# Kernel tuning notes

Measured on AMD Instinct MI355X. Metric: run time of the kernel, lower is better.

## Reference

```python
import jax, jax.numpy as jnp
import numpy as np

D_MODEL = 1024
N_HEADS = 16
HEAD_DIM = D_MODEL // N_HEADS


def setup_inputs() -> dict:
    key = jax.random.key(0)
    ks = jax.random.split(key, 5)
    B, S = 4, 2048
    scale = 1.0 / np.sqrt(D_MODEL)
    return {
        "x": jax.random.normal(ks[0], (B, S, D_MODEL), dtype=jnp.float32),
        "wq": jax.random.normal(ks[1], (D_MODEL, D_MODEL), dtype=jnp.float32) * scale,
        "wk": jax.random.normal(ks[2], (D_MODEL, D_MODEL), dtype=jnp.float32) * scale,
        "wv": jax.random.normal(ks[3], (D_MODEL, D_MODEL), dtype=jnp.float32) * scale,
        "wo": jax.random.normal(ks[4], (D_MODEL, D_MODEL), dtype=jnp.float32) * scale,
    }


def reference(x, wq, wk, wv, wo):
    B, S, _ = x.shape
    # projections: x @ W.T, then split heads -> [B, H, S, hd]
    def split_heads(t):
        return t.reshape(B, S, N_HEADS, HEAD_DIM).transpose(0, 2, 1, 3)

    q = split_heads(x @ wq.T)
    k = split_heads(x @ wk.T)
    v = split_heads(x @ wv.T)

    # scores [B, H, S, S], causal mask, stable softmax
    score = jnp.einsum("bhqd,bhkd->bhqk", q, k) / np.sqrt(HEAD_DIM)
    causal = jnp.tril(jnp.ones((S, S), dtype=bool))
    score = jnp.where(causal, score, -jnp.inf)
    attn = jax.nn.softmax(score, axis=-1)

    out = jnp.einsum("bhqk,bhkd->bhqd", attn, v)
    out = out.transpose(0, 2, 1, 3).reshape(B, S, D_MODEL)
    return out @ wo.T
```

## Files before the change

kernel.cpp:

```cpp
#include <hip/hip_runtime.h>
#include <type_traits>


typedef unsigned short u16;
typedef __attribute__((ext_vector_type(8))) short s8;
typedef __attribute__((ext_vector_type(4))) float f4;

#if __has_builtin(__builtin_amdgcn_exp2f)
#define EXP2(x) __builtin_amdgcn_exp2f(x)
#else
#define EXP2(x) exp2f(x)
#endif

__device__ __forceinline__ u16 f2bf(float f) {
    union { float f; unsigned u; } v; v.f = f;
    unsigned r = v.u + 0x7fffu + ((v.u >> 16) & 1u);
    return (u16)(r >> 16);
}

__device__ __forceinline__ unsigned pack_bf2(float a, float b) {
    return __builtin_amdgcn_perm(__float_as_uint(b), __float_as_uint(a),
                                 0x07060302u);
}

__device__ __forceinline__ void cp16(const void* g, void* l) {
    __builtin_amdgcn_global_load_lds(
        (const __attribute__((address_space(1))) unsigned int*)g,
        (__attribute__((address_space(3))) unsigned int*)l, 16, 0, 0);
}

__device__ __forceinline__ s8 load8f(const float* p) {
    const float4 lo = *(const float4*)p;
    const float4 hi = *(const float4*)(p + 4);
    s8 r;
    r[0] = (short)f2bf(lo.x); r[1] = (short)f2bf(lo.y);
    r[2] = (short)f2bf(lo.z); r[3] = (short)f2bf(lo.w);
    r[4] = (short)f2bf(hi.x); r[5] = (short)f2bf(hi.y);
    r[6] = (short)f2bf(hi.z); r[7] = (short)f2bf(hi.w);
    return r;
}

__global__ __launch_bounds__(256)
void f32_to_bf16(const float* __restrict__ in, u16* __restrict__ out, int n8)
{
    const int i = blockIdx.x * 256 + threadIdx.x;
    if (i < n8) *(s8*)(out + (size_t)i * 8) = load8f(in + (size_t)i * 8);
}

__global__ __launch_bounds__(256)
void cvt_xw(const float* __restrict__ x,
            const float* __restrict__ wq, const float* __restrict__ wk,
            const float* __restrict__ wv,
            u16* __restrict__ Xb, u16* __restrict__ Wqkv)
{
    const int i = blockIdx.x * 256 + threadIdx.x;
    if (i < 1048576) {
        *(s8*)(Xb + (size_t)i * 8) = load8f(x + (size_t)i * 8);
    } else {
        const int j = i - 1048576;
        const int sel = j >> 17;
        const int wi  = j & 131071;
        const float* src = (sel == 0) ? wq : ((sel == 1) ? wk : wv);
        *(s8*)(Wqkv + (size_t)sel * 1048576 + (size_t)wi * 8) =
            load8f(src + (size_t)wi * 8);
    }
}

template<typename TC>
__global__ __launch_bounds__(256)
void gemm_bb(const u16* __restrict__ A,
             const u16* __restrict__ W0, const u16* __restrict__ W1,
             const u16* __restrict__ W2,
             TC* __restrict__ C0, TC* __restrict__ C1,
             u16* __restrict__ VT, int K, float cscale)
{
    __shared__ u16 As[3][128 * 32];
    __shared__ u16 Bs[3][128 * 32];

    const int t  = threadIdx.x;
    const int bm = blockIdx.x;
    const int nglob = blockIdx.y * 128;

    const u16* W; int nloc, mode;
    if (nglob < 1024)      { W = W0; nloc = nglob;        mode = 0; }
    else if (nglob < 2048) { W = W1; nloc = nglob - 1024; mode = 1; }
    else                   { W = W2; nloc = nglob - 2048; mode = 2; }

    const int lane = t & 63, w = t >> 6;
    const int wm = (w >> 1) * 64, wn = (w & 1) * 64;
    const int quad = lane >> 4, l16 = lane & 15;

    const int sc = (((lane & 3) ^ ((lane >> 3) & 3))) * 8;
    const int sr = w * 32 + (lane >> 2);
    const u16* Ag0 = A + (size_t)(bm * 128 + sr) * K + sc;
    const u16* Ag1 = Ag0 + (size_t)16 * K;
    const u16* Wg0 = W + (size_t)(nloc + sr) * K + sc;
    const u16* Wg1 = Wg0 + (size_t)16 * K;
    const int la0 = (w * 32) * 32;
    const int la1 = (w * 32 + 16) * 32;

    const int ca = (quad ^ ((l16 >> 1) & 3)) * 8;

    auto stage = [&](int buf, int k0) {
        cp16(Ag0 + k0, &As[buf][la0]);
        cp16(Ag1 + k0, &As[buf][la1]);
        cp16(Wg0 + k0, &Bs[buf][la0]);
        cp16(Wg1 + k0, &Bs[buf][la1]);
    };

    f4 acc[4][4];
    for (int i = 0; i < 4; i++)
        for (int j = 0; j < 4; j++)
            acc[i][j] = (f4){0.f, 0.f, 0.f, 0.f};

    stage(0, 0);
    stage(1, 32);
    int cur = 0;
    for (int k0 = 0; k0 < K; k0 += 32) {
        if (k0 + 32 < K) asm volatile("s_waitcnt vmcnt(4)" ::: "memory");
        else             asm volatile("s_waitcnt vmcnt(0)" ::: "memory");
        __builtin_amdgcn_s_barrier();
        if (k0 + 96 <= K) stage((cur + 2) % 3, k0 + 64);

        s8 af[4], bf[4];
        for (int i = 0; i < 4; i++)
            af[i] = *(const s8*)&As[cur][(wm + i * 16 + l16) * 32 + ca];
        for (int j = 0; j < 4; j++)
            bf[j] = *(const s8*)&Bs[cur][(wn + j * 16 + l16) * 32 + ca];
        for (int i = 0; i < 4; i++)
            for (int j = 0; j < 4; j++)
                acc[i][j] = __builtin_amdgcn_mfma_f32_16x16x32_bf16(
                                af[i], bf[j], acc[i][j], 0, 0, 0);
        cur = (cur == 2) ? 0 : cur + 1;
    }

    if (mode == 2) {
        for (int i = 0; i < 4; i++) {
            const int row0 = bm * 128 + wm + i * 16 + quad * 4;
            const int b = row0 >> 11, s = row0 & 2047;
            for (int j = 0; j < 4; j++) {
                const int n = nloc + wn + j * 16 + l16;
                const int h = n >> 6, d = n & 63;
                unsigned lo = ((unsigned)f2bf(acc[i][j][1]) << 16) | f2bf(acc[i][j][0]);
                unsigned hi = ((unsigned)f2bf(acc[i][j][3]) << 16) | f2bf(acc[i][j][2]);
                *(uint2*)(VT + ((size_t)((b * 16 + h) * 64 + d)) * 2048 + s) =
                    make_uint2(lo, hi);
            }
        }
    } else {
        TC* C = (mode == 0) ? C0 : C1;
        const float cs = (mode == 0) ? cscale : 1.0f;
        for (int i = 0; i < 4; i++) {
            const int row = bm * 128 + wm + i * 16 + quad * 4;
            for (int j = 0; j < 4; j++) {
                const int col = nloc + wn + j * 16 + l16;
                for (int r = 0; r < 4; r++) {
                    const float val = acc[i][j][r] * cs;
                    if constexpr (std::is_same<TC, float>::value)
                        C[(size_t)(row + r) * 1024 + col] = val;
                    else
                        C[(size_t)(row + r) * 1024 + col] = f2bf(val);
                }
            }
        }
    }
}

#define PSTR 72

__global__ __launch_bounds__(512)
void attn8(const u16* __restrict__ Q, const u16* __restrict__ K,
           const u16* __restrict__ Vt, u16* __restrict__ O)
{
    __shared__ u16 Ks[2][64 * 64];
    __shared__ u16 Vs[2][64 * 64];
    __shared__ u16 Ps[8][32 * PSTR];

    const int bh = blockIdx.x;
    const int yy = blockIdx.y;
    const int p  = (yy < 4) ? (7 - yy) : (yy - 4);
    const int h  = bh & 15, b = bh >> 4;

    const int t = threadIdx.x, lane = t & 63, w = t >> 6;
    const int quad = lane >> 4, l16 = lane & 15;
    const int colH = h * 64;

    const int q32 = 8 * p + w;
    const int ktw = q32 / 2 + 1;
    const int ktb = 4 * p + 4;

    s8 ones;
    for (int e = 0; e < 8; e++) ones[e] = (short)0x3F80;

    const int vrow = lane >> 3;
    const int scc  = ((lane & 7) ^ vrow) * 8;
    const int r0   = w * 8 + vrow;
    const u16* Kg = K  + ((size_t)b * 2048 + r0) * 1024 + colH + scc;
    const u16* Vg = Vt + ((size_t)(b * 16 + h) * 64 + r0) * 2048 + scc;
    const int klds = (w * 8) * 64;

    auto stageKV = [&](int buf, int kt) {
        cp16(Kg + (size_t)kt * 65536, &Ks[buf][klds]);
        cp16(Vg + kt * 64, &Vs[buf][klds]);
    };

    const size_t rowQ0 = (size_t)b * 2048 + q32 * 32;

    s8 qf[2][2];
    for (int i = 0; i < 2; i++)
        for (int kk = 0; kk < 2; kk++)
            qf[i][kk] = *(const s8*)&Q[(rowQ0 + i * 16 + l16) * 1024 +
                                       colH + kk * 32 + quad * 8];

    f4 o_acc[2][4];
    f4 l_acc[2];
    for (int i = 0; i < 2; i++) {
        l_acc[i] = (f4){0.f, 0.f, 0.f, 0.f};
        for (int j = 0; j < 4; j++)
            o_acc[i][j] = (f4){0.f, 0.f, 0.f, 0.f};
    }

    stageKV(0, 0);
    int cur = 0;

    for (int kt = 0; kt < ktb; ++kt) {
        __syncthreads();
        if (kt + 1 < ktb) stageKV(cur ^ 1, kt + 1);

        if (kt < ktw) {
            f4 sa[4][2];
            for (int j = 0; j < 4; j++)
                for (int i = 0; i < 2; i++)
                    sa[j][i] = (f4){0.f, 0.f, 0.f, 0.f};
            for (int kk = 0; kk < 2; kk++) {
                s8 kf[4];
                for (int j = 0; j < 4; j++)
                    kf[j] = *(const s8*)&Ks[cur][(j * 16 + l16) * 64 +
                                            (((kk * 4 + quad) ^ (l16 & 7)) * 8)];
                for (int j = 0; j < 4; j++)
                    for (int i = 0; i < 2; i++)
                        sa[j][i] = __builtin_amdgcn_mfma_f32_16x16x32_bf16(
                                       kf[j], qf[i][kk], sa[j][i], 0, 0, 0);
            }

            const bool diag = (kt == ktw - 1);
            for (int i = 0; i < 2; i++) {
                const int q_l = i * 16 + l16;
                const int q_g = q32 * 32 + q_l;
                for (int j = 0; j < 4; j++) {
                    const int kv0 = kt * 64 + j * 16 + quad * 4;
                    float p0 = EXP2(sa[j][i][0]);
                    float p1 = EXP2(sa[j][i][1]);
                    float p2 = EXP2(sa[j][i][2]);
                    float p3 = EXP2(sa[j][i][3]);
                    if (diag) {
                        if (kv0 + 0 > q_g) p0 = 0.f;
                        if (kv0 + 1 > q_g) p1 = 0.f;
                        if (kv0 + 2 > q_g) p2 = 0.f;
                        if (kv0 + 3 > q_g) p3 = 0.f;
                    }
                    *(uint2*)&Ps[w][q_l * PSTR + j * 16 + quad * 4] =
                        make_uint2(pack_bf2(p0, p1), pack_bf2(p2, p3));
                }
            }

            for (int kk = 0; kk < 2; kk++) {
                s8 pf[2], vf[4];
                for (int i = 0; i < 2; i++)
                    pf[i] = *(const s8*)&Ps[w][(i * 16 + l16) * PSTR +
                                               kk * 32 + quad * 8];
                for (int jd = 0; jd < 4; jd++)
                    vf[jd] = *(const s8*)&Vs[cur][(jd * 16 + l16) * 64 +
                                            (((kk * 4 + quad) ^ (l16 & 7)) * 8)];
                for (int i = 0; i < 2; i++)
                    l_acc[i] = __builtin_amdgcn_mfma_f32_16x16x32_bf16(
                                   pf[i], ones, l_acc[i], 0, 0, 0);
                for (int i = 0; i < 2; i++)
                    for (int jd = 0; jd < 4; jd++)
                        o_acc[i][jd] = __builtin_amdgcn_mfma_f32_16x16x32_bf16(
                                           pf[i], vf[jd], o_acc[i][jd], 0, 0, 0);
            }
        }
        cur ^= 1;
    }

    for (int i = 0; i < 2; i++) {
        float rinv[4];
        for (int r = 0; r < 4; r++) rinv[r] = 1.0f / l_acc[i][r];
        for (int jd = 0; jd < 4; jd++)
            for (int r = 0; r < 4; r++) {
                const size_t row = rowQ0 + i * 16 + quad * 4 + r;
                O[row * 1024 + colH + jd * 16 + l16] =
                    f2bf(o_acc[i][jd][r] * rinv[r]);
            }
    }
}

extern "C" void kernel_launch(void* const* d_in, const int* in_sizes, int n_in,
                              void* d_out, int out_size, void* d_ws, size_t ws_size,
                              hipStream_t stream)
{
    const float* x  = (const float*)d_in[0];
    const float* wq = (const float*)d_in[1];
    const float* wk = (const float*)d_in[2];
    const float* wv = (const float*)d_in[3];
    const float* wo = (const float*)d_in[4];
    float* out = (float*)d_out;

    const size_t MD = (size_t)8192 * 1024;
    const size_t WD = (size_t)1024 * 1024;
    u16* Qb  = (u16*)d_ws;
    u16* Kb  = Qb + MD;
    u16* Vtb = Kb + MD;
    u16* Xb  = Vtb + MD;
    u16* Wqkv = (u16*)d_out;
    u16* Ob  = Qb;
    u16* Wob = Kb;

    cvt_xw<<<5632, 256, 0, stream>>>(x, wq, wk, wv, Xb, Wqkv);

    gemm_bb<u16><<<dim3(64, 24), 256, 0, stream>>>(
        Xb, Wqkv, Wqkv + WD, Wqkv + 2 * WD, Qb, Kb, Vtb, 1024, 0.18033688f);

    attn8<<<dim3(64, 8), 512, 0, stream>>>(Qb, Kb, Vtb, Ob);

    f32_to_bf16<<<512, 256, 0, stream>>>(wo, Wob, (int)(WD / 8));

    gemm_bb<float><<<dim3(64, 8), 256, 0, stream>>>(
        Ob, Wob, Wob, Wob, out, out, nullptr, 1024, 1.0f);
}
```

Baseline: 242.6 us.

## Rewrite projection GEMMs as 8-wave 128x256 tiles with ping-pong staged pipeline

Replaces the 256-thread 128x128 GEMM with a 512-thread kernel that computes 128x256 tiles. The K loop works in 64-wide steps split into half-stages that are double-buffered. MFMA bursts are interleaved with LDS reads and async global-to-LDS copies, separated by barriers and raised wave priority during the MFMA bursts. The aim is to reuse each A tile across more columns and to hide load latency behind matrix math. The cost is more LDS per block, more barriers per iteration, and fewer blocks in the grid, which may leave the output projection under-filling the GPU.

Measured after the change: 254.9 us. 1.05x slower.

```diff
diff --git a/kernel.cpp b/kernel.cpp
--- a/kernel.cpp
+++ b/kernel.cpp
@@ -67,19 +67,19 @@
 }
 
 template<typename TC>
-__global__ __launch_bounds__(256)
-void gemm_bb(const u16* __restrict__ A,
-             const u16* __restrict__ W0, const u16* __restrict__ W1,
-             const u16* __restrict__ W2,
-             TC* __restrict__ C0, TC* __restrict__ C1,
-             u16* __restrict__ VT, int K, float cscale)
-{
-    __shared__ u16 As[3][128 * 32];
-    __shared__ u16 Bs[3][128 * 32];
+__global__ __launch_bounds__(512)
+void gemm8p(const u16* __restrict__ A,
+            const u16* __restrict__ W0, const u16* __restrict__ W1,
+            const u16* __restrict__ W2,
+            TC* __restrict__ C0, TC* __restrict__ C1,
+            u16* __restrict__ VT, int K, float cscale)
+{
+    __shared__ u16 As[2][2][128 * 32];
+    __shared__ u16 Bs[2][2][256 * 32];
 
     const int t  = threadIdx.x;
     const int bm = blockIdx.x;
-    const int nglob = blockIdx.y * 128;
+    const int nglob = blockIdx.y * 256;
 
     const u16* W; int nloc, mode;
     if (nglob < 1024)      { W = W0; nloc = nglob;        mode = 0; }
@@ -87,59 +87,123 @@
     else                   { W = W2; nloc = nglob - 2048; mode = 2; }
 
     const int lane = t & 63, w = t >> 6;
-    const int wm = (w >> 1) * 64, wn = (w & 1) * 64;
+    const int wr = w >> 2, wc = w & 3;
     const int quad = lane >> 4, l16 = lane & 15;
 
-    const int sc = (((lane & 3) ^ ((lane >> 3) & 3))) * 8;
-    const int sr = w * 32 + (lane >> 2);
-    const u16* Ag0 = A + (size_t)(bm * 128 + sr) * K + sc;
-    const u16* Ag1 = Ag0 + (size_t)16 * K;
-    const u16* Wg0 = W + (size_t)(nloc + sr) * K + sc;
-    const u16* Wg1 = Wg0 + (size_t)16 * K;
-    const int la0 = (w * 32) * 32;
-    const int la1 = (w * 32 + 16) * 32;
+    const int sw = ((lane & 3) ^ ((lane >> 3) & 3)) * 8;
+    const int r16 = lane >> 2;
+    const u16* Ag = A + (size_t)(bm * 128 + 16 * w + r16) * K + sw;
+    const u16* Wg = W + (size_t)(nloc + 32 * w + r16) * K + sw;
+    const int ldsA = (16 * w) * 32;
+    const int ldsB0 = (32 * w) * 32;
+    const int ldsB1 = (32 * w + 16) * 32;
+
+    auto stageH = [&](int buf, int kt, int hf) {
+        const int k0 = kt * 64 + hf * 32;
+        cp16(Ag + k0, &As[buf][hf][ldsA]);
+        cp16(Wg + k0, &Bs[buf][hf][ldsB0]);
+        cp16(Wg + (size_t)16 * K + k0, &Bs[buf][hf][ldsB1]);
+    };
 
     const int ca = (quad ^ ((l16 >> 1) & 3)) * 8;
-
-    auto stage = [&](int buf, int k0) {
-        cp16(Ag0 + k0, &As[buf][la0]);
-        cp16(Ag1 + k0, &As[buf][la1]);
-        cp16(Wg0 + k0, &Bs[buf][la0]);
-        cp16(Wg1 + k0, &Bs[buf][la1]);
-    };
+    #define ARD(i, kk) (*(const s8*)&As[cur][kk][(wr * 64 + (i) * 16 + l16) * 32 + ca])
+    #define BRD(j, kk) (*(const s8*)&Bs[cur][kk][(wc * 64 + (j) * 16 + l16) * 32 + ca])
 
     f4 acc[4][4];
+    #pragma unroll
     for (int i = 0; i < 4; i++)
+        #pragma unroll
         for (int j = 0; j < 4; j++)
             acc[i][j] = (f4){0.f, 0.f, 0.f, 0.f};
 
-    stage(0, 0);
-    stage(1, 32);
+    const int NK = K >> 6;
+    stageH(0, 0, 0);
+    stageH(0, 0, 1);
+    stageH(1, 1, 0);
+    asm volatile("s_waitcnt vmcnt(6)" ::: "memory");
+    __builtin_amdgcn_s_barrier();
+
     int cur = 0;
-    for (int k0 = 0; k0 < K; k0 += 32) {
-        if (k0 + 32 < K) asm volatile("s_waitcnt vmcnt(4)" ::: "memory");
-        else             asm volatile("s_waitcnt vmcnt(0)" ::: "memory");
-        __builtin_amdgcn_s_barrier();
-        if (k0 + 96 <= K) stage((cur + 2) % 3, k0 + 64);
-
+    for (int kt = 0; kt < NK; ++kt) {
+        const bool m1 = (kt + 1 < NK);
+        const bool m2 = (kt + 2 < NK);
         s8 af[4], bf[4];
-        for (int i = 0; i < 4; i++)
-            af[i] = *(const s8*)&As[cur][(wm + i * 16 + l16) * 32 + ca];
-        for (int j = 0; j < 4; j++)
-            bf[j] = *(const s8*)&Bs[cur][(wn + j * 16 + l16) * 32 + ca];
-        for (int i = 0; i < 4; i++)
+
+        #pragma unroll
+        for (int i = 0; i < 2; i++) af[i] = ARD(i, 0);
+        #pragma unroll
+        for (int j = 0; j < 4; j++) bf[j] = BRD(j, 0);
+        if (m1) stageH(cur ^ 1, kt + 1, 1);
+        __builtin_amdgcn_s_barrier();
+        __builtin_amdgcn_s_setprio(1);
+        #pragma unroll
+        for (int i = 0; i < 2; i++)
+            #pragma unroll
             for (int j = 0; j < 4; j++)
                 acc[i][j] = __builtin_amdgcn_mfma_f32_16x16x32_bf16(
                                 af[i], bf[j], acc[i][j], 0, 0, 0);
-        cur = (cur == 2) ? 0 : cur + 1;
-    }
+        __builtin_amdgcn_s_setprio(0);
+        __builtin_amdgcn_s_barrier();
+
+        #pragma unroll
+        for (int i = 2; i < 4; i++) af[i] = ARD(i, 0);
+        __builtin_amdgcn_s_barrier();
+        __builtin_amdgcn_s_setprio(1);
+        #pragma unroll
+        for (int i = 2; i < 4; i++)
+            #pragma unroll
+            for (int j = 0; j < 4; j++)
+                acc[i][j] = __builtin_amdgcn_mfma_f32_16x16x32_bf16(
+                                af[i], bf[j], acc[i][j], 0, 0, 0);
+        __builtin_amdgcn_s_setprio(0);
+        if (m1) asm volatile("s_waitcnt vmcnt(6)" ::: "memory");
+        else    asm volatile("s_waitcnt vmcnt(0)" ::: "memory");
+        __builtin_amdgcn_s_barrier();
+
+        #pragma unroll
+        for (int i = 0; i < 2; i++) af[i] = ARD(i, 1);
+        #pragma unroll
+        for (int j = 0; j < 4; j++) bf[j] = BRD(j, 1);
+        if (m2) stageH(cur, kt + 2, 0);
+        __builtin_amdgcn_s_barrier();
+        __builtin_amdgcn_s_setprio(1);
+        #pragma unroll
+        for (int i = 0; i < 2; i++)
+            #pragma unroll
+            for (int j = 0; j < 4; j++)
+                acc[i][j] = __builtin_amdgcn_mfma_f32_16x16x32_bf16(
+                                af[i], bf[j], acc[i][j], 0, 0, 0);
+        __builtin_amdgcn_s_setprio(0);
+        __builtin_amdgcn_s_barrier();
+
+        #pragma unroll
+        for (int i = 2; i < 4; i++) af[i] = ARD(i, 1);
+        __builtin_amdgcn_s_barrier();
+        __builtin_amdgcn_s_setprio(1);
+        #pragma unroll
+        for (int i = 2; i < 4; i++)
+            #pragma unroll
+            for (int j = 0; j < 4; j++)
+                acc[i][j] = __builtin_amdgcn_mfma_f32_16x16x32_bf16(
+                                af[i], bf[j], acc[i][j], 0, 0, 0);
+        __builtin_amdgcn_s_setprio(0);
+        if (m2)      asm volatile("s_waitcnt vmcnt(6)" ::: "memory");
+        else if (m1) asm volatile("s_waitcnt vmcnt(3)" ::: "memory");
+        __builtin_amdgcn_s_barrier();
+
+        cur ^= 1;
+    }
+    #undef ARD
+    #undef BRD
 
     if (mode == 2) {
+        #pragma unroll
         for (int i = 0; i < 4; i++) {
-            const int row0 = bm * 128 + wm + i * 16 + quad * 4;
+            const int row0 = bm * 128 + wr * 64 + i * 16 + quad * 4;
             const int b = row0 >> 11, s = row0 & 2047;
+            #pragma unroll
             for (int j = 0; j < 4; j++) {
-                const int n = nloc + wn + j * 16 + l16;
+                const int n = nloc + wc * 64 + j * 16 + l16;
                 const int h = n >> 6, d = n & 63;
                 unsigned lo = ((unsigned)f2bf(acc[i][j][1]) << 16) | f2bf(acc[i][j][0]);
                 unsigned hi = ((unsigned)f2bf(acc[i][j][3]) << 16) | f2bf(acc[i][j][2]);
@@ -150,10 +214,13 @@
     } else {
         TC* C = (mode == 0) ? C0 : C1;
         const float cs = (mode == 0) ? cscale : 1.0f;
+        #pragma unroll
         for (int i = 0; i < 4; i++) {
-            const int row = bm * 128 + wm + i * 16 + quad * 4;
+            const int row = bm * 128 + wr * 64 + i * 16 + quad * 4;
+            #pragma unroll
             for (int j = 0; j < 4; j++) {
-                const int col = nloc + wn + j * 16 + l16;
+                const int col = nloc + wc * 64 + j * 16 + l16;
+                #pragma unroll
                 for (int r = 0; r < 4; r++) {
                     const float val = acc[i][j][r] * cs;
                     if constexpr (std::is_same<TC, float>::value)
@@ -319,13 +386,13 @@
 
     cvt_xw<<<5632, 256, 0, stream>>>(x, wq, wk, wv, Xb, Wqkv);
 
-    gemm_bb<u16><<<dim3(64, 24), 256, 0, stream>>>(
+    gemm8p<u16><<<dim3(64, 12), 512, 0, stream>>>(
         Xb, Wqkv, Wqkv + WD, Wqkv + 2 * WD, Qb, Kb, Vtb, 1024, 0.18033688f);
 
     attn8<<<dim3(64, 8), 512, 0, stream>>>(Qb, Kb, Vtb, Ob);
 
     f32_to_bf16<<<512, 256, 0, stream>>>(wo, Wob, (int)(WD / 8));
 
-    gemm_bb<float><<<dim3(64, 8), 256, 0, stream>>>(
+    gemm8p<float><<<dim3(64, 4), 512, 0, stream>>>(
         Ob, Wob, Wob, Wob, out, out, nullptr, 1024, 1.0f);
 }
```
